# Optimization experiments

Hardware: AMD Instinct MI355X
Metric: run time of the kernel (lower is better)

The kernel has to match this reference:

```python
import jax, jax.numpy as jnp
import numpy as np
from jax import lax

N, C, H, W = 32, 256, 56, 56
SHIFT = 2  # p_5_1_0, frozen random.randint(-3,3)

def setup_inputs() -> dict:
    key = jax.random.key(0)
    k1, k2, k3 = jax.random.split(key, 3)
    x = jax.random.normal(k1, (N, C, H, W), dtype=jnp.float32)
    w6 = jax.random.normal(k2, (C, 1), dtype=jnp.float32) * 0.1  # trunc_normal(std=0.1) approx
    w7 = jax.random.normal(k3, (C, C * 25), dtype=jnp.float32) * (1.0 / np.sqrt(C * 25))
    return {"x": x, "w6": w6, "w7": w7}

def reference(x, w6, w7):
    # t_1: max over width -> (n,c,h)
    t1 = jnp.max(x, axis=3)
    # t_3/t_4: relu then tanh
    t4 = jnp.tanh(jax.nn.relu(x))
    # t_5: roll along height axis
    t5 = jnp.roll(x, SHIFT, axis=2)
    # t_6: einsum 'abcd,be->aecd' with e=1 -> (n,h,w)
    t6 = jnp.einsum('nchw,c->nhw', t4, w6[:, 0])
    # t_2 + p_7: unfold(5x5, dilation=3, padding=6) + 1x1 conv == dilated 5x5 conv.
    # unfold channel ordering is c*25 + (kh*5+kw), so reshape to OIHW directly.
    conv_w = w7.reshape(C, C, 5, 5)
    t7 = lax.conv_general_dilated(
        x, conv_w, window_strides=(1, 1), padding=[(6, 6), (6, 6)],
        rhs_dilation=(3, 3), dimension_numbers=('NCHW', 'OIHW', 'NCHW'))
    t8 = x * t7
    # t_9: softmax over width of (n,h,w)
    t9 = jax.nn.softmax(t6, axis=2)
    t10 = t9[:, None, :, :] * t5
    t11 = t10 + t8
    return t1[:, :, :, None] - t11
```

## Files before the change

kernel.cpp:

```cpp
#include <hip/hip_runtime.h>
#include <hip/hip_bf16.h>
#include <math.h>

typedef __bf16 bf16x8 __attribute__((ext_vector_type(8)));
typedef short  s16x8  __attribute__((ext_vector_type(8)));
typedef float  f32x4  __attribute__((ext_vector_type(4)));
typedef unsigned short u16;

#define NN 32
#define CC 256
#define HH 56
#define WW 56
#define HP 68
#define XP2_BYTES 75759616ull
#define XP2_OFF 0ull
#define WT3_OFF 75759616ull
#define T1_OFF  79036416ull
#define T9_OFF  80871424ull

__device__ inline u16 f2bf(float f) {
    unsigned int u = __builtin_bit_cast(unsigned int, f);
    u = (u + 0x7fffu + ((u >> 16) & 1u)) >> 16;
    return (u16)u;
}

__device__ inline void gl_lds16(const char* g, char* l) {
    __builtin_amdgcn_global_load_lds(
        (const __attribute__((address_space(1))) unsigned int*)g,
        (__attribute__((address_space(3))) unsigned int*)l, 16, 0, 0);
}

__global__ void zero_xp2(u16* __restrict__ xp2, size_t n16) {
    size_t i = (size_t)blockIdx.x * blockDim.x + threadIdx.x;
    size_t stride = (size_t)gridDim.x * blockDim.x;
    uint4* p = (uint4*)xp2;
    uint4 z; z.x = z.y = z.z = z.w = 0u;
    for (; i < n16; i += stride) p[i] = z;
}

__global__ __launch_bounds__(256)
void pack_x(const float* __restrict__ x, u16* __restrict__ xp2) {
    int nh = blockIdx.x;
    int n = nh / HH, h = nh % HH;
    int lane = threadIdx.x & 63, wv = threadIdx.x >> 6;
    if (lane >= WW) return;
    const float* src = x + (size_t)n * (CC * HH * WW) + h * WW + lane;
    u16* dst = xp2 + (((size_t)n * HP + (h + 6)) * HP + (lane + 6)) * CC;
    for (int oct = wv; oct < 32; oct += 4) {
        s16x8 pk;
#pragma unroll
        for (int j = 0; j < 8; ++j)
            pk[j] = (short)f2bf(src[(size_t)(oct * 8 + j) * (HH * WW)]);
        *(s16x8*)(dst + oct * 8) = pk;
    }
}

__global__ __launch_bounds__(256)
void pack_w(const float* __restrict__ w7, u16* __restrict__ wt3) {
    int idx = blockIdx.x * 256 + threadIdx.x;
    int c_out = idx / 6400;
    int k = idx - c_out * 6400;
    int cin = k / 25;
    int tap = k - cin * 25;
    int chunk = cin >> 5;
    int ci = cin & 31;
    wt3[(((size_t)(tap * 8 + chunk)) * CC + c_out) * 32 + ci] = f2bf(w7[idx]);
}

__global__ __launch_bounds__(256)
void t169_kernel(const float* __restrict__ x, const float* __restrict__ w6,
                 float* __restrict__ t1, float* __restrict__ t9) {
    const int n = blockIdx.x / HH;
    const int h = blockIdx.x % HH;
    const int wave = threadIdx.x >> 6;
    const int lane = threadIdx.x & 63;
    const bool valid = lane < WW;
    const int wl = valid ? lane : (WW - 1);
    const float* xrow = x + ((size_t)(n * CC) * HH + h) * WW;
    float accw = 0.f;
    __shared__ float sbuf[4 * 64];
    for (int i = 0; i < 64; ++i) {
        int c = wave * 64 + i;
        float xv = xrow[(size_t)c * (HH * WW) + wl];
        float xm = valid ? xv : -INFINITY;
#pragma unroll
        for (int off = 32; off > 0; off >>= 1)
            xm = fmaxf(xm, __shfl_xor(xm, off));
        if (lane == 0) t1[(size_t)(n * CC + c) * HH + h] = xm;
        if (valid) accw += tanhf(fmaxf(xv, 0.f)) * w6[c];
    }
    sbuf[wave * 64 + lane] = accw;
    __syncthreads();
    if (wave == 0) {
        float s = sbuf[lane] + sbuf[64 + lane] + sbuf[128 + lane] + sbuf[192 + lane];
        float sm = valid ? s : -INFINITY;
        float mx = sm;
#pragma unroll
        for (int off = 32; off > 0; off >>= 1)
            mx = fmaxf(mx, __shfl_xor(mx, off));
        float e = valid ? expf(s - mx) : 0.f;
        float tot = e;
#pragma unroll
        for (int off = 32; off > 0; off >>= 1)
            tot += __shfl_xor(tot, off);
        if (valid) t9[((size_t)n * HH + h) * WW + lane] = e / tot;
    }
}

__global__ __launch_bounds__(512, 2)
void conv_main(const char* __restrict__ xp2b, const char* __restrict__ wt3b,
               const float* __restrict__ x, const float* __restrict__ t1,
               const float* __restrict__ t9, float* __restrict__ out) {
    extern __shared__ __align__(16) char smem[];
    const int tile = blockIdx.x;
    const int tid  = threadIdx.x;
    const int wid  = tid >> 6;
    const int lane = tid & 63;
    const int m = lane & 15;
    const int q = lane >> 4;
    const int wr = wid >> 2;
    const int wc = wid & 3;
    const bool isA = wid < 4;

    unsigned vb[4] = {0, 0, 0, 0};
    if (!isA) {
        const int wb = wid - 4;
#pragma unroll
        for (int i = 0; i < 4; ++i) {
            int p = tile * 256 + wb * 64 + i * 16 + (lane >> 2);
            int n = p / (HH * WW);
            int rem = p - n * (HH * WW);
            int hh = rem / WW;
            int ww = rem - hh * WW;
            vb[i] = ((((unsigned)n * HP + hh + 6) * HP) + ww + 6) * 512 + (lane & 3) * 16;
        }
    }

    auto stage2 = [&](int tt, int half) {
        const int kn = (tt < 200) ? tt : (tt - 200);
        char* dst = smem + (size_t)(tt & 3) * 32768;
        if (isA) {
            const char* g = wt3b + (size_t)kn * 16384 + wid * 4096 + half * 2048 + lane * 16;
            char* d = dst + wid * 4096 + half * 2048 + lane * 16;
            gl_lds16(g, d);
            gl_lds16(g + 1024, d + 1024);
        } else {
            const int tp = kn >> 3, ch = kn & 7;
            const char* gb = xp2b +
                (ptrdiff_t)((tp / 5) * 3 - 6) * (HP * 512) +
                (ptrdiff_t)((tp % 5) * 3 - 6) * 512 + ch * 64;
            char* d = dst + 16384 + (wid - 4) * 4096 + half * 2048 + lane * 16;
            gl_lds16(gb + vb[half * 2],     d);
            gl_lds16(gb + vb[half * 2 + 1], d + 1024);
        }
    };

    f32x4 acc[8][4];
#pragma unroll
    for (int mi = 0; mi < 8; ++mi)
#pragma unroll
        for (int ni = 0; ni < 4; ++ni) {
            acc[mi][ni][0] = 0.f; acc[mi][ni][1] = 0.f;
            acc[mi][ni][2] = 0.f; acc[mi][ni][3] = 0.f;
        }

    const int aoff = (wr * 128 + m) * 64 + q * 16;
    const int boff = 16384 + (wc * 64 + m) * 64 + q * 16;

    stage2(0, 0); stage2(0, 1);
    stage2(1, 0); stage2(1, 1);
    stage2(2, 0); stage2(2, 1);
    asm volatile("s_waitcnt vmcnt(8)" ::: "memory");
    __builtin_amdgcn_s_barrier();

    for (int t = 0; t < 200; ++t) {
        const char* bp = smem + (size_t)(t & 3) * 32768;
        bf16x8 av[4], bv[4];

        stage2(t + 3, 0);
#pragma unroll
        for (int ni = 0; ni < 4; ++ni)
            bv[ni] = *(const bf16x8*)(const void*)(bp + boff + ni * 1024);
#pragma unroll
        for (int mi = 0; mi < 4; ++mi)
            av[mi] = *(const bf16x8*)(const void*)(bp + aoff + mi * 1024);
        __builtin_amdgcn_s_setprio(1);
#pragma unroll
        for (int mi = 0; mi < 4; ++mi)
#pragma unroll
            for (int ni = 0; ni < 4; ++ni)
                acc[mi][ni] = __builtin_amdgcn_mfma_f32_16x16x32_bf16(
                    av[mi], bv[ni], acc[mi][ni], 0, 0, 0);
        __builtin_amdgcn_s_setprio(0);
        __builtin_amdgcn_s_barrier();

        stage2(t + 3, 1);
#pragma unroll
        for (int mi = 0; mi < 4; ++mi)
            av[mi] = *(const bf16x8*)(const void*)(bp + aoff + 4096 + mi * 1024);
        __builtin_amdgcn_s_setprio(1);
#pragma unroll
        for (int mi = 0; mi < 4; ++mi)
#pragma unroll
            for (int ni = 0; ni < 4; ++ni)
                acc[mi + 4][ni] = __builtin_amdgcn_mfma_f32_16x16x32_bf16(
                    av[mi], bv[ni], acc[mi + 4][ni], 0, 0, 0);
        __builtin_amdgcn_s_setprio(0);
        asm volatile("s_waitcnt vmcnt(8)" ::: "memory");
        __builtin_amdgcn_s_barrier();
    }

#pragma unroll
    for (int ni = 0; ni < 4; ++ni) {
        const int p = tile * 256 + wc * 64 + ni * 16 + m;
        const int n = p / (HH * WW);
        const int rem = p - n * (HH * WW);
        const int h = rem / WW;
        const int w = rem - h * WW;
        const float t9v = t9[((size_t)n * HH + h) * WW + w];
        const int hprev = (h >= 2) ? (h - 2) : (h + HH - 2);
#pragma unroll
        for (int mi = 0; mi < 8; ++mi) {
            const int c = wr * 128 + mi * 16 + q * 4;
#pragma unroll
            for (int r = 0; r < 4; ++r) {
                const size_t rowi = (size_t)(n * CC + c + r) * HH;
                const float t1v = t1[rowi + h];
                const float xv = x[(rowi + h) * WW + w];
                const float xr = x[(rowi + hprev) * WW + w];
                out[(rowi + h) * WW + w] = t1v - (t9v * xr + xv * acc[mi][ni][r]);
            }
        }
    }
}

extern "C" void kernel_launch(void* const* d_in, const int* in_sizes, int n_in,
                              void* d_out, int out_size, void* d_ws, size_t ws_size,
                              hipStream_t stream) {
    const float* x  = (const float*)d_in[0];
    const float* w6 = (const float*)d_in[1];
    const float* w7 = (const float*)d_in[2];
    float* out = (float*)d_out;
    char* ws = (char*)d_ws;
    u16*   xp2 = (u16*)(ws + XP2_OFF);
    u16*   wt3 = (u16*)(ws + WT3_OFF);
    float* t1  = (float*)(ws + T1_OFF);
    float* t9  = (float*)(ws + T9_OFF);

    static bool lds_cfg_done = false;
    if (!lds_cfg_done) {
        (void)hipFuncSetAttribute((const void*)conv_main,
                                  hipFuncAttributeMaxDynamicSharedMemorySize,
                                  131072);
        lds_cfg_done = true;
    }

    zero_xp2<<<dim3(2048), dim3(256), 0, stream>>>(xp2, XP2_BYTES / 16);
    pack_x<<<dim3(NN * HH), dim3(256), 0, stream>>>(x, xp2);
    pack_w<<<dim3(6400), dim3(256), 0, stream>>>(w7, wt3);
    t169_kernel<<<dim3(NN * HH), dim3(256), 0, stream>>>(x, w6, t1, t9);
    conv_main<<<dim3(392), dim3(512), 131072, stream>>>((const char*)xp2, (const char*)wt3,
                                                        x, t1, t9, out);
}
```

Baseline: 692.7 us.

## Fuse x packing into prep kernel, zero only halo, reorder LDS layout

Packing x to padded NHWC bf16 now happens inside the t1/t9 prep kernel through an LDS transpose buffer, so x is read once instead of twice. Only the halo of the padded buffer is zeroed instead of the whole buffer. Weights and input rows are laid out so each lane's MFMA fragment sits contiguously in LDS (lane*16 offsets), which avoids bank conflicts. Conv tiles are also remapped across blocks to improve cache locality. The cost is extra LDS in the prep kernel (about 29KB), which may lower its occupancy.

```diff
diff --git a/kernel.cpp b/kernel.cpp
--- a/kernel.cpp
+++ b/kernel.cpp
@@ -30,28 +30,21 @@
         (__attribute__((address_space(3))) unsigned int*)l, 16, 0, 0);
 }
 
-__global__ void zero_xp2(u16* __restrict__ xp2, size_t n16) {
-    size_t i = (size_t)blockIdx.x * blockDim.x + threadIdx.x;
-    size_t stride = (size_t)gridDim.x * blockDim.x;
-    uint4* p = (uint4*)xp2;
+__global__ void zero_halo(u16* __restrict__ xp2) {
+    const int total = NN * 1488 * 32;
+    int i = blockIdx.x * blockDim.x + threadIdx.x;
+    const int stride = gridDim.x * blockDim.x;
     uint4 z; z.x = z.y = z.z = z.w = 0u;
-    for (; i < n16; i += stride) p[i] = z;
-}
-
-__global__ __launch_bounds__(256)
-void pack_x(const float* __restrict__ x, u16* __restrict__ xp2) {
-    int nh = blockIdx.x;
-    int n = nh / HH, h = nh % HH;
-    int lane = threadIdx.x & 63, wv = threadIdx.x >> 6;
-    if (lane >= WW) return;
-    const float* src = x + (size_t)n * (CC * HH * WW) + h * WW + lane;
-    u16* dst = xp2 + (((size_t)n * HP + (h + 6)) * HP + (lane + 6)) * CC;
-    for (int oct = wv; oct < 32; oct += 4) {
-        s16x8 pk;
-#pragma unroll
-        for (int j = 0; j < 8; ++j)
-            pk[j] = (short)f2bf(src[(size_t)(oct * 8 + j) * (HH * WW)]);
-        *(s16x8*)(dst + oct * 8) = pk;
+    for (; i < total; i += stride) {
+        int chunk = i & 31;
+        int pid = i >> 5;
+        int n = pid / 1488;
+        int hp = pid - n * 1488;
+        int row, col;
+        if (hp < 816) { int r = hp / 68; col = hp - r * 68; row = (r < 6) ? r : r + 56; }
+        else { int hq = hp - 816; int rr = hq / 12; int c12 = hq - rr * 12;
+               row = 6 + rr; col = (c12 < 6) ? c12 : c12 + 56; }
+        *(uint4*)((char*)xp2 + ((((size_t)n * HP + row) * HP + col) * 512) + chunk * 16) = z;
     }
 }
 
@@ -62,14 +55,17 @@
     int k = idx - c_out * 6400;
     int cin = k / 25;
     int tap = k - cin * 25;
-    int chunk = cin >> 5;
+    int kn = tap * 8 + (cin >> 5);
     int ci = cin & 31;
-    wt3[(((size_t)(tap * 8 + chunk)) * CC + c_out) * 32 + ci] = f2bf(w7[idx]);
+    int wr = c_out >> 7, mi = (c_out >> 4) & 7, mrow = c_out & 15;
+    int q = ci >> 3, j = ci & 7;
+    wt3[(size_t)kn * 8192 + wr * 4096 + mi * 512 + (q * 16 + mrow) * 8 + j] = f2bf(w7[idx]);
 }
 
 __global__ __launch_bounds__(256)
-void t169_kernel(const float* __restrict__ x, const float* __restrict__ w6,
-                 float* __restrict__ t1, float* __restrict__ t9) {
+void prep_kernel(const float* __restrict__ x, const float* __restrict__ w6,
+                 float* __restrict__ t1, float* __restrict__ t9,
+                 u16* __restrict__ xp2) {
     const int n = blockIdx.x / HH;
     const int h = blockIdx.x % HH;
     const int wave = threadIdx.x >> 6;
@@ -79,9 +75,11 @@
     const float* xrow = x + ((size_t)(n * CC) * HH + h) * WW;
     float accw = 0.f;
     __shared__ float sbuf[4 * 64];
+    __shared__ u16 xbuf[WW * 260];
     for (int i = 0; i < 64; ++i) {
         int c = wave * 64 + i;
         float xv = xrow[(size_t)c * (HH * WW) + wl];
+        if (valid) xbuf[lane * 260 + c] = f2bf(xv);
         float xm = valid ? xv : -INFINITY;
 #pragma unroll
         for (int off = 32; off > 0; off >>= 1)
@@ -105,6 +103,15 @@
             tot += __shfl_xor(tot, off);
         if (valid) t9[((size_t)n * HH + h) * WW + lane] = e / tot;
     }
+    u16* dst = xp2 + (((size_t)n * HP + h + 6) * HP + 6) * CC;
+    for (int id = threadIdx.x; id < WW * 32; id += 256) {
+        int p = id >> 5, oct = id & 31;
+        const u16* srcl = xbuf + p * 260 + oct * 8;
+        uint2 a = *(const uint2*)srcl;
+        uint2 b = *(const uint2*)(srcl + 4);
+        uint4 v; v.x = a.x; v.y = a.y; v.z = b.x; v.w = b.y;
+        *(uint4*)(dst + (size_t)p * CC + oct * 8) = v;
+    }
 }
 
 __global__ __launch_bounds__(512, 2)
@@ -112,7 +119,8 @@
                const float* __restrict__ x, const float* __restrict__ t1,
                const float* __restrict__ t9, float* __restrict__ out) {
     extern __shared__ __align__(16) char smem[];
-    const int tile = blockIdx.x;
+    const int bid = blockIdx.x;
+    const int tile = (bid & 7) * 49 + (bid >> 3);
     const int tid  = threadIdx.x;
     const int wid  = tid >> 6;
     const int lane = tid & 63;
@@ -127,12 +135,12 @@
         const int wb = wid - 4;
 #pragma unroll
         for (int i = 0; i < 4; ++i) {
-            int p = tile * 256 + wb * 64 + i * 16 + (lane >> 2);
+            int p = tile * 256 + wb * 64 + i * 16 + m;
             int n = p / (HH * WW);
             int rem = p - n * (HH * WW);
             int hh = rem / WW;
             int ww = rem - hh * WW;
-            vb[i] = ((((unsigned)n * HP + hh + 6) * HP) + ww + 6) * 512 + (lane & 3) * 16;
+            vb[i] = ((((unsigned)n * HP + hh + 6) * HP) + ww + 6) * 512 + q * 16;
         }
     }
 
@@ -164,8 +172,8 @@
             acc[mi][ni][2] = 0.f; acc[mi][ni][3] = 0.f;
         }
 
-    const int aoff = (wr * 128 + m) * 64 + q * 16;
-    const int boff = 16384 + (wc * 64 + m) * 64 + q * 16;
+    const int aoff = wr * 8192 + lane * 16;
+    const int boff = 16384 + wc * 4096 + lane * 16;
 
     stage2(0, 0); stage2(0, 1);
     stage2(1, 0); stage2(1, 1);
@@ -255,10 +263,9 @@
         lds_cfg_done = true;
     }
 
-    zero_xp2<<<dim3(2048), dim3(256), 0, stream>>>(xp2, XP2_BYTES / 16);
-    pack_x<<<dim3(NN * HH), dim3(256), 0, stream>>>(x, xp2);
+    zero_halo<<<dim3(1024), dim3(256), 0, stream>>>(xp2);
     pack_w<<<dim3(6400), dim3(256), 0, stream>>>(w7, wt3);
-    t169_kernel<<<dim3(NN * HH), dim3(256), 0, stream>>>(x, w6, t1, t9);
+    prep_kernel<<<dim3(NN * HH), dim3(256), 0, stream>>>(x, w6, t1, t9, xp2);
     conv_main<<<dim3(392), dim3(512), 131072, stream>>>((const char*)xp2, (const char*)wt3,
                                                         x, t1, t9, out);
 }
```

Measured after the change: 756.0 us. 9.1% more time.
